# Kernel tuning notes

Measured on AMD Instinct MI355X. Metric: run time of the kernel, lower is better.

## Reference

```python
import jax, jax.numpy as jnp
import numpy as np

N_NODES = 50000


def graph_conv(src, dst, x, W, b, n_nodes):
    """DGL GraphConv, norm='both': D_out^{-1/2} A D_in^{-1/2} x W + b.
    src/dst: [E] edge endpoints (message flows src -> dst).
    """
    ones = jnp.ones(src.shape[0], dtype=x.dtype)
    deg_out = jnp.clip(jax.ops.segment_sum(ones, src, num_segments=n_nodes), 1.0)
    deg_in = jnp.clip(jax.ops.segment_sum(ones, dst, num_segments=n_nodes), 1.0)
    h = x * jax.lax.rsqrt(deg_out)[:, None]          # src-side normalization
    msgs = h[src]                                     # [E, F] gather (irregular)
    agg = jax.ops.segment_sum(msgs, dst, num_segments=n_nodes)  # SpMM scatter-add
    agg = agg * jax.lax.rsqrt(deg_in)[:, None]        # dst-side normalization
    return agg @ W + b


def setup_inputs() -> dict:
    key = jax.random.key(0)
    ks = jax.random.split(key, 9)
    E = 600000
    in_f, hid, emb = 128, 64, 32
    features = jax.random.normal(ks[0], (N_NODES, in_f), dtype=jnp.float32)
    src = jax.random.randint(ks[1], (E,), 0, N_NODES)
    dst = jax.random.randint(ks[2], (E,), 0, N_NODES)

    def glorot(k, fan_in, fan_out):
        lim = np.sqrt(6.0 / (fan_in + fan_out)).astype(np.float32)
        return jax.random.uniform(k, (fan_in, fan_out), jnp.float32, -lim, lim)

    return {
        "features": features, "src": src, "dst": dst,
        "W1": glorot(ks[3], in_f, hid), "b1": jnp.zeros((hid,), jnp.float32),
        "W2": glorot(ks[4], hid, emb), "b2": jnp.zeros((emb,), jnp.float32),
        "W3": glorot(ks[5], emb, in_f), "b3": jnp.zeros((in_f,), jnp.float32),
    }


def reference(features, src, dst, W1, b1, W2, b2, W3, b3):
    h = jax.nn.relu(graph_conv(src, dst, features, W1, b1, N_NODES))
    z = graph_conv(src, dst, h, W2, b2, N_NODES)
    recon = graph_conv(src, dst, z, W3, b3, N_NODES)
    return (z, recon)
```

## Files before the change

kernel.cpp:

```cpp
#include <hip/hip_runtime.h>
#include <hip/hip_bf16.h>


#define NN   50000
#define HPS  32
#define HPD  128
#define FNB  2
#define FBIN 25000
typedef unsigned short u16;
typedef unsigned char  u8;
typedef __attribute__((ext_vector_type(8))) short bf16x8;
typedef __attribute__((ext_vector_type(4))) float f32x4;

__device__ __forceinline__ float bfhi(unsigned u) {
    unsigned v = u & 0xFFFF0000u;
    return __builtin_bit_cast(float, v);
}
__device__ __forceinline__ float bflo(unsigned u) {
    unsigned v = u << 16;
    return __builtin_bit_cast(float, v);
}
__device__ __forceinline__ unsigned f2bf(float f) {
    unsigned u = __builtin_bit_cast(unsigned, f);
    return (u + 0x7FFFu + ((u >> 16) & 1u)) >> 16;
}

__global__ __launch_bounds__(256) void k_hist1(
    const int* __restrict__ src, const int* __restrict__ dst,
    u8* __restrict__ slab, int E, int slice_s, int slice_d)
{
    __shared__ unsigned h[NN / 4];
    const bool is_src = blockIdx.x < HPS;
    const int p       = is_src ? blockIdx.x : blockIdx.x - HPS;
    const int slice   = is_src ? slice_s : slice_d;
    const int* __restrict__ idx = is_src ? src : dst;

    for (int i = threadIdx.x; i < NN / 4; i += 256) h[i] = 0;
    __syncthreads();

    const int beg = p * slice;
    const int fin = min(beg + slice, E);
    for (int i = beg + threadIdx.x * 4; i + 3 < fin; i += 1024) {
        const int4 v = *(const int4*)(idx + i);
        atomicAdd(&h[v.x >> 2], 1u << ((v.x & 3) << 3));
        atomicAdd(&h[v.y >> 2], 1u << ((v.y & 3) << 3));
        atomicAdd(&h[v.z >> 2], 1u << ((v.z & 3) << 3));
        atomicAdd(&h[v.w >> 2], 1u << ((v.w & 3) << 3));
    }
    for (int i = beg + ((fin - beg) & ~3) + threadIdx.x; i < fin; i += 256) {
        const int u = idx[i];
        atomicAdd(&h[u >> 2], 1u << ((u & 3) << 3));
    }
    __syncthreads();

    unsigned* out = (unsigned*)(slab + (size_t)blockIdx.x * NN);
    for (int i = threadIdx.x; i < NN / 4; i += 256) out[i] = h[i];
}

__global__ __launch_bounds__(256) void k_reduce_scan(
    u8* __restrict__ slab, float* __restrict__ rs_out, float* __restrict__ rs_in,
    int* __restrict__ partial, int* __restrict__ blocksum, u8* __restrict__ pad4,
    unsigned* __restrict__ csr_words, int ncw, int N)
{
    __shared__ int tmp[256];
    const int tid = threadIdx.x;
    const int i = blockIdx.x * 256 + tid;

    int run = 0;
    if (i < N) {
        const u8* s_src = slab + i;
        u8*       s_dst = slab + (size_t)HPS * NN + i;
        int so = 0;
#pragma unroll 8
        for (int p = 0; p < HPS; ++p) so += s_src[(size_t)p * NN];
#pragma unroll 8
        for (int p = 0; p < HPD; ++p) {
            const int c = s_dst[(size_t)p * NN];
            s_dst[(size_t)p * NN] = (u8)run;
            run += c;
        }
        rs_out[i] = rsqrtf(fmaxf((float)so, 1.0f));
        rs_in[i]  = rsqrtf(fmaxf((float)run, 1.0f));
    }
    const int pad = (run + 15) & ~15;
    if (i < N) pad4[i] = (u8)(pad >> 2);
    tmp[tid] = pad; __syncthreads();
    for (int off = 1; off < 256; off <<= 1) {
        int t = (tid >= off) ? tmp[tid - off] : 0;
        __syncthreads(); tmp[tid] += t; __syncthreads();
    }
    if (i < N) partial[i] = tmp[tid];
    if (tid == 255) blocksum[blockIdx.x] = tmp[255];

    for (int w = blockIdx.x * 256 + tid; w < ncw; w += gridDim.x * 256)
        csr_words[w] = 0xC350C350u;
}

__global__ __launch_bounds__(256) void k_scan23(
    const int* __restrict__ partial, const int* __restrict__ blocksum,
    const u8* __restrict__ pad4, uint2* __restrict__ seg, int n, int nb)
{
    __shared__ int tmp[256];
    const int tid = threadIdx.x;
    int v = (tid < nb) ? blocksum[tid] : 0;
    tmp[tid] = v; __syncthreads();
    for (int off = 1; off < 256; off <<= 1) {
        int t = (tid >= off) ? tmp[tid - off] : 0;
        __syncthreads(); tmp[tid] += t; __syncthreads();
    }
    __syncthreads();
    const int i = blockIdx.x * 256 + tid;
    if (i < n) {
        const int base = (blockIdx.x > 0) ? tmp[blockIdx.x - 1] : 0;
        const int incl = partial[i] + base;
        const unsigned q = pad4[i];
        seg[i] = make_uint2((unsigned)(incl - (int)(q << 2)), q);
    }
}

__global__ __launch_bounds__(256) void k_fill2(
    const int* __restrict__ src, const int* __restrict__ dst,
    const uint2* __restrict__ seg, const u8* __restrict__ slab,
    u16* __restrict__ csr, int E, int slice, int N)
{
    __shared__ int cur[FBIN];
    const int bin = blockIdx.x / HPD;
    const int p   = blockIdx.x % HPD;
    const int lo  = bin * FBIN;

    const u8* part_off = slab + (size_t)(HPS + p) * NN;
    for (int j = threadIdx.x; j < FBIN; j += 256) {
        const int node = lo + j;
        cur[j] = (int)seg[node].x + (int)part_off[node];
    }
    __syncthreads();

    const int beg = p * slice;
    const int fin = min(beg + slice, E);
    for (int i = beg + threadIdx.x * 4; i + 3 < fin; i += 1024) {
        const int4 d = *(const int4*)(dst + i);
        const int4 s = *(const int4*)(src + i);
        int u;
        u = d.x - lo; if ((unsigned)u < (unsigned)FBIN) csr[atomicAdd(&cur[u], 1)] = (u16)s.x;
        u = d.y - lo; if ((unsigned)u < (unsigned)FBIN) csr[atomicAdd(&cur[u], 1)] = (u16)s.y;
        u = d.z - lo; if ((unsigned)u < (unsigned)FBIN) csr[atomicAdd(&cur[u], 1)] = (u16)s.z;
        u = d.w - lo; if ((unsigned)u < (unsigned)FBIN) csr[atomicAdd(&cur[u], 1)] = (u16)s.w;
    }
    for (int i = beg + ((fin - beg) & ~3) + threadIdx.x; i < fin; i += 256) {
        int u = dst[i] - lo;
        if ((unsigned)u < (unsigned)FBIN) csr[atomicAdd(&cur[u], 1)] = (u16)src[i];
    }
}

#define XS1 136
__global__ __launch_bounds__(256) void k_gemm_mfma_A(
    const float* __restrict__ X, const float* __restrict__ W1,
    const float* __restrict__ rs, u16* __restrict__ Y,
    u16* __restrict__ t2b, u16* __restrict__ zb, int N)
{
    __shared__ u16 sXb[64 * XS1];
    __shared__ u16 sWt[64 * XS1];
    const int tid = threadIdx.x;
    const int m0 = blockIdx.x * 64;

    if (blockIdx.x == 0) {
        if (tid < 32)      ((unsigned*)(Y   + (size_t)NN * 64))[tid]      = 0;
        else if (tid < 48) ((unsigned*)(t2b + (size_t)NN * 32))[tid - 32] = 0;
        else if (tid < 64) ((unsigned*)(zb  + (size_t)NN * 32))[tid - 48] = 0;
    }

    for (int i = tid; i < 128 * 64; i += 256) {
        const int k = i >> 6, n = i & 63;
        sWt[n * XS1 + k] = (u16)f2bf(W1[i]);
    }
    for (int i = tid; i < 64 * 32; i += 256) {
        const int r  = i >> 5;
        const int c4 = (i & 31) * 4;
        const int gr = m0 + r;
        float4 v = make_float4(0.f, 0.f, 0.f, 0.f);
        if (gr < N) v = *(const float4*)(X + (size_t)gr * 128 + c4);
        uint2 pk;
        pk.x = f2bf(v.x) | (f2bf(v.y) << 16);
        pk.y = f2bf(v.z) | (f2bf(v.w) << 16);
        *(uint2*)(sXb + r * XS1 + c4) = pk;
    }
    __syncthreads();

    const int wv   = tid >> 6;
    const int lane = tid & 63;
    const int l15  = lane & 15;
    const int quad = lane >> 4;

    f32x4 acc[4] = {};
    const u16* ax = sXb + (wv * 16 + l15) * XS1 + quad * 8;
    const u16* bx = sWt + l15 * XS1 + quad * 8;
#pragma unroll
    for (int ks = 0; ks < 4; ++ks) {
        const bf16x8 af = *(const bf16x8*)(ax + ks * 32);
#pragma unroll
        for (int nt = 0; nt < 4; ++nt) {
            const bf16x8 bf = *(const bf16x8*)(bx + nt * 16 * XS1 + ks * 32);
            acc[nt] = __builtin_amdgcn_mfma_f32_16x16x32_bf16(af, bf, acc[nt], 0, 0, 0);
        }
    }

    const int mrow = m0 + wv * 16 + quad * 4;
    float sc[4];
#pragma unroll
    for (int r = 0; r < 4; ++r) sc[r] = (mrow + r < N) ? rs[mrow + r] : 0.f;
#pragma unroll
    for (int r = 0; r < 4; ++r) {
        const int gr = mrow + r;
        if (gr < N) {
#pragma unroll
            for (int nt = 0; nt < 4; ++nt)
                Y[(size_t)gr * 64 + nt * 16 + l15] = (u16)f2bf(acc[nt][r] * sc[r]);
        }
    }
}

#define ACC8(q) do { \
    a[0] += bflo((q).x); a[1] += bfhi((q).x); a[2] += bflo((q).y); a[3] += bfhi((q).y); \
    a[4] += bflo((q).z); a[5] += bfhi((q).z); a[6] += bflo((q).w); a[7] += bfhi((q).w); } while (0)

#define GATHER4(SRCB, RW) do { \
    const uint2 w = *(const uint2*)(csr + j); \
    const int s0 = w.x & 0xFFFF, s1 = w.x >> 16; \
    const int s2 = w.y & 0xFFFF, s3 = w.y >> 16; \
    const uint4 q0 = *(const uint4*)(SRCB + (size_t)s0 * RW + c8); \
    const uint4 q1 = *(const uint4*)(SRCB + (size_t)s1 * RW + c8); \
    const uint4 q2 = *(const uint4*)(SRCB + (size_t)s2 * RW + c8); \
    const uint4 q3 = *(const uint4*)(SRCB + (size_t)s3 * RW + c8); \
    ACC8(q0); ACC8(q1); ACC8(q2); ACC8(q3); } while (0)

__global__ __launch_bounds__(256) void k_gather_gemm_B(
    const uint2* __restrict__ seg, const u16* __restrict__ csr,
    const u16* __restrict__ t1b, const float* __restrict__ rs_in,
    const float* __restrict__ rs_out, const float* __restrict__ b1,
    const float* __restrict__ W2, u16* __restrict__ t2b, int N)
{
    __shared__ float sh[32][72];
    __shared__ float sW[64 * 32];
    const int tid = threadIdx.x;

    for (int i = tid; i < 64 * 32 / 4; i += 256)
        ((float4*)sW)[i] = ((const float4*)W2)[i];

    const int nb   = tid >> 5;
    const int sub  = tid & 31;
    const int qtr  = sub >> 3;
    const int c8   = (sub & 7) * 8;

    uint2 sgs[4];
#pragma unroll
    for (int b = 0; b < 4; ++b) {
        const int node = blockIdx.x * 32 + b * 8 + nb;
        sgs[b] = (node < N) ? seg[node] : make_uint2(0u, 0u);
    }

#pragma unroll
    for (int b = 0; b < 4; ++b) {
        const int nloc = b * 8 + nb;
        const int node = blockIdx.x * 32 + nloc;
        float a[8];
#pragma unroll
        for (int t = 0; t < 8; ++t) a[t] = 0.f;
        const int j0 = (int)sgs[b].x + qtr * (int)sgs[b].y;
        const int j1 = j0 + (int)sgs[b].y;
        for (int j = j0; j < j1; j += 4) GATHER4(t1b, 64);
#pragma unroll
        for (int t = 0; t < 8; ++t) {
            a[t] += __shfl_xor(a[t], 8);
            a[t] += __shfl_xor(a[t], 16);
        }
        if (node < N && qtr == 0) {
            const float rs = rs_in[node];
#pragma unroll
            for (int t = 0; t < 8; ++t)
                sh[nloc][c8 + t] = fmaxf(a[t] * rs + b1[c8 + t], 0.f);
        }
    }
    __syncthreads();

    const int n2 = tid >> 3;
    const int c4 = (tid & 7) * 4;
    float4 acc = make_float4(0.f, 0.f, 0.f, 0.f);
#pragma unroll 8
    for (int k = 0; k < 64; ++k) {
        const float xv = sh[n2][k];
        const float4 w = *(const float4*)(sW + k * 32 + c4);
        acc.x += xv * w.x; acc.y += xv * w.y; acc.z += xv * w.z; acc.w += xv * w.w;
    }
    const int gn = blockIdx.x * 32 + n2;
    if (gn < N) {
        const float s = rs_out[gn];
        uint2 pk;
        pk.x = f2bf(acc.x * s) | (f2bf(acc.y * s) << 16);
        pk.y = f2bf(acc.z * s) | (f2bf(acc.w * s) << 16);
        *(uint2*)(t2b + (size_t)gn * 32 + c4) = pk;
    }
}

__global__ __launch_bounds__(256) void k_gather_C(
    const uint2* __restrict__ seg, const u16* __restrict__ csr,
    const u16* __restrict__ t2b, const float* __restrict__ rs_in,
    const float* __restrict__ rs_out, const float* __restrict__ b2,
    float* __restrict__ z, u16* __restrict__ zb, int N)
{
    const int node = blockIdx.x * 16 + (threadIdx.x >> 4);
    const int sub  = threadIdx.x & 15;
    const int qtr  = sub >> 2;
    const int c8   = (sub & 3) * 8;
    if (node >= N) return;

    const uint2 sg = seg[node];
    const int j0 = (int)sg.x + qtr * (int)sg.y;
    const int j1 = j0 + (int)sg.y;

    float a[8];
#pragma unroll
    for (int t = 0; t < 8; ++t) a[t] = 0.f;
    for (int j = j0; j < j1; j += 4) GATHER4(t2b, 32);

#pragma unroll
    for (int t = 0; t < 8; ++t) {
        a[t] += __shfl_xor(a[t], 4);
        a[t] += __shfl_xor(a[t], 8);
    }
    if (qtr) return;

    const float rs = rs_in[node];
    float v[8];
#pragma unroll
    for (int t = 0; t < 8; ++t) v[t] = a[t] * rs + b2[c8 + t];

    float* o = z + (size_t)node * 32 + c8;
    *(float4*)(o)     = make_float4(v[0], v[1], v[2], v[3]);
    *(float4*)(o + 4) = make_float4(v[4], v[5], v[6], v[7]);

    const float ss = rs_out[node];
    uint4 pk;
    pk.x = f2bf(v[0] * ss) | (f2bf(v[1] * ss) << 16);
    pk.y = f2bf(v[2] * ss) | (f2bf(v[3] * ss) << 16);
    pk.z = f2bf(v[4] * ss) | (f2bf(v[5] * ss) << 16);
    pk.w = f2bf(v[6] * ss) | (f2bf(v[7] * ss) << 16);
    *(uint4*)(zb + (size_t)node * 32 + c8) = pk;
}

__global__ __launch_bounds__(256) void k_gather_gemm_D(
    const uint2* __restrict__ seg, const u16* __restrict__ csr,
    const u16* __restrict__ zb, const float* __restrict__ rs_in,
    const float* __restrict__ W3, const float* __restrict__ b3,
    float* __restrict__ recon, int N)
{
    __shared__ float sa[32][36];
    __shared__ float sW[32 * 128];
    const int tid = threadIdx.x;

    for (int i = tid; i < 32 * 128 / 4; i += 256)
        ((float4*)sW)[i] = ((const float4*)W3)[i];

    const int nb   = tid >> 4;
    const int sub  = tid & 15;
    const int qtr  = sub >> 2;
    const int c8   = (sub & 3) * 8;

    uint2 sgs[2];
#pragma unroll
    for (int b = 0; b < 2; ++b) {
        const int node = blockIdx.x * 32 + b * 16 + nb;
        sgs[b] = (node < N) ? seg[node] : make_uint2(0u, 0u);
    }

#pragma unroll
    for (int b = 0; b < 2; ++b) {
        const int nloc = b * 16 + nb;
        const int node = blockIdx.x * 32 + nloc;
        float a[8];
#pragma unroll
        for (int t = 0; t < 8; ++t) a[t] = 0.f;
        const int j0 = (int)sgs[b].x + qtr * (int)sgs[b].y;
        const int j1 = j0 + (int)sgs[b].y;
        for (int j = j0; j < j1; j += 4) GATHER4(zb, 32);
#pragma unroll
        for (int t = 0; t < 8; ++t) {
            a[t] += __shfl_xor(a[t], 4);
            a[t] += __shfl_xor(a[t], 8);
        }
        if (node < N && qtr == 0) {
            const float rs = rs_in[node];
#pragma unroll
            for (int t = 0; t < 8; ++t) sa[nloc][c8 + t] = a[t] * rs;
        }
    }
    __syncthreads();

    const int ng = (tid >> 5) * 4;
    const int c4 = (tid & 31) * 4;
    const float4 bb = *(const float4*)(b3 + c4);
    float4 acc[4];
#pragma unroll
    for (int i = 0; i < 4; ++i) acc[i] = bb;
#pragma unroll 4
    for (int k = 0; k < 32; ++k) {
        const float4 w = *(const float4*)(sW + k * 128 + c4);
#pragma unroll
        for (int i = 0; i < 4; ++i) {
            const float xv = sa[ng + i][k];
            acc[i].x += xv * w.x; acc[i].y += xv * w.y;
            acc[i].z += xv * w.z; acc[i].w += xv * w.w;
        }
    }
#pragma unroll
    for (int i = 0; i < 4; ++i) {
        const int gn = blockIdx.x * 32 + ng + i;
        if (gn < N) *(float4*)(recon + (size_t)gn * 128 + c4) = acc[i];
    }
}

extern "C" void kernel_launch(void* const* d_in, const int* in_sizes, int n_in,
                              void* d_out, int out_size, void* d_ws, size_t ws_size,
                              hipStream_t stream) {
    const float* feat = (const float*)d_in[0];
    const int*   src  = (const int*)d_in[1];
    const int*   dst  = (const int*)d_in[2];
    const float* W1   = (const float*)d_in[3];
    const float* b1   = (const float*)d_in[4];
    const float* W2   = (const float*)d_in[5];
    const float* b2   = (const float*)d_in[6];
    const float* W3   = (const float*)d_in[7];
    const float* b3   = (const float*)d_in[8];

    const int E = in_sizes[1];
    const int N = in_sizes[0] / 128;
    const int slice_s = (((E + HPS - 1) / HPS) + 3) & ~3;
    const int slice_d = (((E + HPD - 1) / HPD) + 3) & ~3;
    const int CSRMAX = E + 15 * N;
    const int ncw = CSRMAX / 2;

    const size_t SLABB = (size_t)(HPS + HPD) * NN;
    u8*  slab     = (u8*)d_ws;
    uint2* seg    = (uint2*)(slab + SLABB);
    int* scan_p   = (int*)(seg + N + 16);
    int* blocksum = scan_p + N;
    u16* csr      = (u16*)(blocksum + 256);
    float* rs_out = (float*)(csr + CSRMAX);
    float* rs_in  = rs_out + N;
    u16* t2b      = (u16*)(rs_in + N);
    u16* zb       = t2b + (size_t)(N + 8) * 32;
    u8*  pad4     = (u8*)(zb + (size_t)(N + 8) * 32);
    u16* t1b      = (u16*)slab;

    float* z_out  = (float*)d_out;
    float* recon  = z_out + (size_t)N * 32;

    const int B = 256;
    const int nb_scan = (N + 255) / 256;

    k_hist1<<<HPS + HPD, B, 0, stream>>>(src, dst, slab, E, slice_s, slice_d);
    k_reduce_scan<<<nb_scan, B, 0, stream>>>(slab, rs_out, rs_in, scan_p, blocksum,
                                             pad4, (unsigned*)csr, ncw, N);
    k_scan23<<<nb_scan, B, 0, stream>>>(scan_p, blocksum, pad4, seg, N, nb_scan);
    k_fill2<<<FNB * HPD, B, 0, stream>>>(src, dst, seg, slab, csr, E, slice_d, N);

    k_gemm_mfma_A<<<(N + 63) / 64, B, 0, stream>>>(
        feat, W1, rs_out, t1b, t2b, zb, N);

    k_gather_gemm_B<<<(N + 31) / 32, B, 0, stream>>>(
        seg, csr, t1b, rs_in, rs_out, b1, W2, t2b, N);

    k_gather_C<<<(N + 15) / 16, B, 0, stream>>>(
        seg, csr, t2b, rs_in, rs_out, b2, z_out, zb, N);

    k_gather_gemm_D<<<(N + 31) / 32, B, 0, stream>>>(
        seg, csr, zb, rs_in, W3, b3, recon, N);
}
```

Baseline: 182.2 us.

## Split layer-1 bf16 features into two 32-column halves for gather

```diff
diff --git a/kernel.cpp b/kernel.cpp
--- a/kernel.cpp
+++ b/kernel.cpp
@@ -155,7 +155,7 @@
 #define XS1 136
 __global__ __launch_bounds__(256) void k_gemm_mfma_A(
     const float* __restrict__ X, const float* __restrict__ W1,
-    const float* __restrict__ rs, u16* __restrict__ Y,
+    const float* __restrict__ rs, u16* __restrict__ t1lo, u16* __restrict__ t1hi,
     u16* __restrict__ t2b, u16* __restrict__ zb, int N)
 {
     __shared__ u16 sXb[64 * XS1];
@@ -164,9 +164,10 @@
     const int m0 = blockIdx.x * 64;
 
     if (blockIdx.x == 0) {
-        if (tid < 32)      ((unsigned*)(Y   + (size_t)NN * 64))[tid]      = 0;
-        else if (tid < 48) ((unsigned*)(t2b + (size_t)NN * 32))[tid - 32] = 0;
-        else if (tid < 64) ((unsigned*)(zb  + (size_t)NN * 32))[tid - 48] = 0;
+        if (tid < 16)      ((unsigned*)(t1lo + (size_t)NN * 32))[tid]      = 0;
+        else if (tid < 32) ((unsigned*)(t1hi + (size_t)NN * 32))[tid - 16] = 0;
+        else if (tid < 48) ((unsigned*)(t2b  + (size_t)NN * 32))[tid - 32] = 0;
+        else if (tid < 64) ((unsigned*)(zb   + (size_t)NN * 32))[tid - 48] = 0;
     }
 
     for (int i = tid; i < 128 * 64; i += 256) {
@@ -212,9 +213,10 @@
     for (int r = 0; r < 4; ++r) {
         const int gr = mrow + r;
         if (gr < N) {
-#pragma unroll
-            for (int nt = 0; nt < 4; ++nt)
-                Y[(size_t)gr * 64 + nt * 16 + l15] = (u16)f2bf(acc[nt][r] * sc[r]);
+            t1lo[(size_t)gr * 32 +  0 + l15] = (u16)f2bf(acc[0][r] * sc[r]);
+            t1lo[(size_t)gr * 32 + 16 + l15] = (u16)f2bf(acc[1][r] * sc[r]);
+            t1hi[(size_t)gr * 32 +  0 + l15] = (u16)f2bf(acc[2][r] * sc[r]);
+            t1hi[(size_t)gr * 32 + 16 + l15] = (u16)f2bf(acc[3][r] * sc[r]);
         }
     }
 }
@@ -235,9 +237,10 @@
 
 __global__ __launch_bounds__(256) void k_gather_gemm_B(
     const uint2* __restrict__ seg, const u16* __restrict__ csr,
-    const u16* __restrict__ t1b, const float* __restrict__ rs_in,
-    const float* __restrict__ rs_out, const float* __restrict__ b1,
-    const float* __restrict__ W2, u16* __restrict__ t2b, int N)
+    const u16* __restrict__ t1lo, const u16* __restrict__ t1hi,
+    const float* __restrict__ rs_in, const float* __restrict__ rs_out,
+    const float* __restrict__ b1, const float* __restrict__ W2,
+    u16* __restrict__ t2b, int N)
 {
     __shared__ float sh[32][72];
     __shared__ float sW[64 * 32];
@@ -246,38 +249,43 @@
     for (int i = tid; i < 64 * 32 / 4; i += 256)
         ((float4*)sW)[i] = ((const float4*)W2)[i];
 
-    const int nb   = tid >> 5;
-    const int sub  = tid & 31;
-    const int qtr  = sub >> 3;
-    const int c8   = (sub & 7) * 8;
-
-    uint2 sgs[4];
-#pragma unroll
-    for (int b = 0; b < 4; ++b) {
-        const int node = blockIdx.x * 32 + b * 8 + nb;
+    const int nb   = tid >> 4;
+    const int sub  = tid & 15;
+    const int qtr  = sub >> 2;
+    const int c8   = (sub & 3) * 8;
+
+    uint2 sgs[2];
+#pragma unroll
+    for (int b = 0; b < 2; ++b) {
+        const int node = blockIdx.x * 32 + b * 16 + nb;
         sgs[b] = (node < N) ? seg[node] : make_uint2(0u, 0u);
     }
 
 #pragma unroll
-    for (int b = 0; b < 4; ++b) {
-        const int nloc = b * 8 + nb;
-        const int node = blockIdx.x * 32 + nloc;
-        float a[8];
-#pragma unroll
-        for (int t = 0; t < 8; ++t) a[t] = 0.f;
-        const int j0 = (int)sgs[b].x + qtr * (int)sgs[b].y;
-        const int j1 = j0 + (int)sgs[b].y;
-        for (int j = j0; j < j1; j += 4) GATHER4(t1b, 64);
-#pragma unroll
-        for (int t = 0; t < 8; ++t) {
-            a[t] += __shfl_xor(a[t], 8);
-            a[t] += __shfl_xor(a[t], 16);
-        }
-        if (node < N && qtr == 0) {
-            const float rs = rs_in[node];
-#pragma unroll
-            for (int t = 0; t < 8; ++t)
-                sh[nloc][c8 + t] = fmaxf(a[t] * rs + b1[c8 + t], 0.f);
+    for (int ph = 0; ph < 2; ++ph) {
+        const u16* __restrict__ tab = ph ? t1hi : t1lo;
+#pragma unroll
+        for (int b = 0; b < 2; ++b) {
+            const int nloc = b * 16 + nb;
+            const int node = blockIdx.x * 32 + nloc;
+            float a[8];
+#pragma unroll
+            for (int t = 0; t < 8; ++t) a[t] = 0.f;
+            const int j0 = (int)sgs[b].x + qtr * (int)sgs[b].y;
+            const int j1 = j0 + (int)sgs[b].y;
+            for (int j = j0; j < j1; j += 4) GATHER4(tab, 32);
+#pragma unroll
+            for (int t = 0; t < 8; ++t) {
+                a[t] += __shfl_xor(a[t], 4);
+                a[t] += __shfl_xor(a[t], 8);
+            }
+            if (node < N && qtr == 0) {
+                const float rs = rs_in[node];
+                const int cc = ph * 32 + c8;
+#pragma unroll
+                for (int t = 0; t < 8; ++t)
+                    sh[nloc][cc + t] = fmaxf(a[t] * rs + b1[cc + t], 0.f);
+            }
         }
     }
     __syncthreads();
@@ -449,7 +457,8 @@
     u16* t2b      = (u16*)(rs_in + N);
     u16* zb       = t2b + (size_t)(N + 8) * 32;
     u8*  pad4     = (u8*)(zb + (size_t)(N + 8) * 32);
-    u16* t1b      = (u16*)slab;
+    u16* t1lo     = (u16*)slab;
+    u16* t1hi     = t1lo + (size_t)(NN + 8) * 32;
 
     float* z_out  = (float*)d_out;
     float* recon  = z_out + (size_t)N * 32;
@@ -464,10 +473,10 @@
     k_fill2<<<FNB * HPD, B, 0, stream>>>(src, dst, seg, slab, csr, E, slice_d, N);
 
     k_gemm_mfma_A<<<(N + 63) / 64, B, 0, stream>>>(
-        feat, W1, rs_out, t1b, t2b, zb, N);
+        feat, W1, rs_out, t1lo, t1hi, t2b, zb, N);
 
     k_gather_gemm_B<<<(N + 31) / 32, B, 0, stream>>>(
-        seg, csr, t1b, rs_in, rs_out, b1, W2, t2b, N);
+        seg, csr, t1lo, t1hi, rs_in, rs_out, b1, W2, t2b, N);
 
     k_gather_C<<<(N + 15) / 16, B, 0, stream>>>(
         seg, csr, t2b, rs_in, rs_out, b2, z_out, zb, N);
```

Result: no change. 184.9 us (+1.5%).
